# Optimization experiments

Hardware: AMD Instinct MI355X
Metric: run time of the kernel (lower is better)

## Reference

```python
import jax, jax.numpy as jnp
import numpy as np
from jax import lax

# Paraformer-large streaming decoder dims
L, H, DFF, NH, DK, K, V, T, S, CKV, LB = 16, 512, 2048, 4, 128, 11, 8404, 64, 2048, 256, 256


def _ln(x, g, b, eps=1e-5):
    m = jnp.mean(x, axis=-1, keepdims=True)
    var = jnp.mean((x - m) ** 2, axis=-1, keepdims=True)
    return (x - m) * lax.rsqrt(var + eps) * g + b


def setup_inputs() -> dict:
    key = jax.random.key(0)
    ks = jax.random.split(key, 20)
    w = lambda k, shp: jax.random.normal(k, shp, jnp.float32) * 0.02
    return {
        "encoder_out": jax.random.normal(ks[0], (1, S, H), jnp.float32),
        "list_frame": jax.random.normal(ks[1], (1, T, H), jnp.float32),
        "fsmn_cache": jax.random.normal(ks[2], (L, 1, H, K - 1), jnp.float32),
        "key_cache": jax.random.normal(ks[3], (L, NH, DK, CKV), jnp.float32),
        "value_cache": jax.random.normal(ks[4], (L, NH, CKV, DK), jnp.float32),
        "norm1_g": jnp.ones((L, H)), "norm1_b": jnp.zeros((L, H)),
        "norm2_g": jnp.ones((L, H)), "norm2_b": jnp.zeros((L, H)),
        "norm3_g": jnp.ones((L, H)), "norm3_b": jnp.zeros((L, H)),
        "ffn_norm_g": jnp.ones((L, DFF)), "ffn_norm_b": jnp.zeros((L, DFF)),
        "w1": w(ks[5], (L, H, DFF)), "b1": jnp.zeros((L, DFF)),
        "w2": w(ks[6], (L, DFF, H)),  # bias-free in FunASR DecoderSANM
        "fsmn_w": w(ks[7], (L, H, K)),  # depthwise conv, groups=H, no bias
        "qw": w(ks[8], (L, H, H)), "qb": jnp.zeros((L, H)),
        "kvw": w(ks[9], (L, H, 2 * H)), "kvb": jnp.zeros((L, 2 * H)),
        "ow": w(ks[10], (L, H, H)), "ob": jnp.zeros((L, H)),
        "d3_norm1_g": jnp.ones((H,)), "d3_norm1_b": jnp.zeros((H,)),
        "d3_w1": w(ks[11], (H, DFF)), "d3_b1": jnp.zeros((DFF,)),
        "d3_ffn_norm_g": jnp.ones((DFF,)), "d3_ffn_norm_b": jnp.zeros((DFF,)),
        "d3_w2": w(ks[12], (DFF, H)),
        "after_norm_g": jnp.ones((H,)), "after_norm_b": jnp.zeros((H,)),
        "out_w": w(ks[13], (H, V)), "out_b": jnp.zeros((V,)),
        "list_frame_len": T,
    }


def reference(encoder_out, list_frame, fsmn_cache, key_cache, value_cache,
              norm1_g, norm1_b, norm2_g, norm2_b, norm3_g, norm3_b,
              ffn_norm_g, ffn_norm_b, w1, b1, w2, fsmn_w, qw, qb, kvw, kvb, ow, ob,
              d3_norm1_g, d3_norm1_b, d3_w1, d3_b1, d3_ffn_norm_g, d3_ffn_norm_b, d3_w2,
              after_norm_g, after_norm_b, out_w, out_b, list_frame_len):
    enc = encoder_out[0]  # [S, H]
    scale = DK ** -0.5

    def layer_fn(lf, p):
        (fc, kc, vc, n1g, n1b, n2g, n2b, n3g, n3b, fng, fnb,
         W1, B1, W2, FW, QW, QB, KVW, KVB, OW, OB) = p
        residual = lf
        y = _ln(lf, n1g, n1b)
        y = _ln(jax.nn.relu(y @ W1 + B1), fng, fnb) @ W2
        y = _ln(y, n2g, n2b)
        # cache concat; slice [look_back:] with look_back = -(K-1)-T keeps all K-1+T cols
        x_cat = jnp.concatenate([fc, jnp.swapaxes(y, 1, 2)], axis=-1)  # [1, H, K-1+T]
        conv = lax.conv_general_dilated(
            x_cat, FW[:, None, :], (1,), 'VALID',
            dimension_numbers=('NCH', 'OIH', 'NCH'), feature_group_count=H)  # [1, H, T]
        x = jnp.swapaxes(conv, 1, 2) + y + residual
        residual = x
        q = (_ln(x, n3g, n3b)[0] @ QW + QB).reshape(-1, NH, DK).transpose(1, 0, 2) * scale  # [h, T, dk]
        kv = enc @ KVW + KVB  # [S, 2H]
        k = kv[:, :H].reshape(-1, NH, DK).transpose(1, 2, 0)  # [h, dk, S]
        v = kv[:, H:].reshape(-1, NH, DK).transpose(1, 0, 2)  # [h, S, dk]
        k = jnp.concatenate([kc, k], axis=2)  # [h, dk, CKV+S]
        v = jnp.concatenate([vc, v], axis=1)  # [h, CKV+S, dk]
        attn = jax.nn.softmax(jnp.einsum('htd,hds->hts', q, k), axis=-1)
        ctx = jnp.einsum('hts,hsd->htd', attn, v).transpose(1, 0, 2).reshape(1, -1, H)
        lf = residual + ctx @ OW + OB
        return lf, (x_cat, k[:, :, -LB:], v[:, -LB:, :])

    layer_params = (fsmn_cache, key_cache, value_cache, norm1_g, norm1_b, norm2_g, norm2_b,
                    norm3_g, norm3_b, ffn_norm_g, ffn_norm_b, w1, b1, w2, fsmn_w,
                    qw, qb, kvw, kvb, ow, ob)
    lf, (save_fsmn, save_keys, save_values) = lax.scan(layer_fn, list_frame, layer_params)
    x = _ln(lf, d3_norm1_g, d3_norm1_b)
    x = _ln(jax.nn.relu(x @ d3_w1 + d3_b1), d3_ffn_norm_g, d3_ffn_norm_b) @ d3_w2
    logits = _ln(x, after_norm_g, after_norm_b) @ out_w + out_b
    max_logit_ids = jnp.argmax(logits, axis=-1).astype(jnp.int32)
    return save_fsmn, save_keys, save_values, max_logit_ids
```

## Files before the change

### kernel.cpp

```cpp
#include <hip/hip_runtime.h>

constexpr int LAY = 16, HID = 512, FF = 2048, NHD = 4, DKH = 128, KW = 11,
              VOC = 8404, TT = 64, SEQ = 2048, LBN = 256;

__global__ void diag_k(float* __restrict__ p, float v) { p[threadIdx.x] = v; }

__global__ __launch_bounds__(256) void redln_k(
    const float* __restrict__ P, int N, int nch,
    const float* __restrict__ bias, const float* __restrict__ res, int relu,
    const float* __restrict__ g, const float* __restrict__ b,
    float* __restrict__ out1, float* __restrict__ out2) {
  __shared__ float buf[2048];
  __shared__ float red[256];
  const int m = blockIdx.x, tid = threadIdx.x;
  float s = 0.f;
  for (int n = tid; n < N; n += 256) {
    const float* p = P + (size_t)m * N + n;
    float v = 0.f;
    for (int c = 0; c < nch; ++c) v += p[(size_t)c * 64 * N];
    if (bias) v += bias[n];
    if (res) v += res[(size_t)m * N + n];
    if (relu) v = fmaxf(v, 0.f);
    if (out1) out1[(size_t)m * N + n] = v;
    buf[n] = v; s += v;
  }
  red[tid] = s; __syncthreads();
  for (int st = 128; st > 0; st >>= 1) { if (tid < st) red[tid] += red[tid + st]; __syncthreads(); }
  const float mean = red[0] / N;
  __syncthreads();
  float vs = 0.f;
  for (int n = tid; n < N; n += 256) { float d = buf[n] - mean; vs += d * d; }
  red[tid] = vs; __syncthreads();
  for (int st = 128; st > 0; st >>= 1) { if (tid < st) red[tid] += red[tid + st]; __syncthreads(); }
  const float inv = rsqrtf(red[0] / N + 1e-5f);
  for (int n = tid; n < N; n += 256)
    out2[(size_t)m * N + n] = (buf[n] - mean) * inv * g[n] + b[n];
}

__global__ __launch_bounds__(256) void gemm_nn(
    const float* __restrict__ A, int lda, long sA,
    const float* __restrict__ B, int ldb, long sB,
    float* __restrict__ C, int ldc, long sC,
    const float* __restrict__ bias,
    const float* __restrict__ res, int ldres,
    int N, int Kd, int flags, int nch,
    float* __restrict__ part, long pzs, int coff,
    int aCh, long aChS) {
  __shared__ float As[64][68];
  __shared__ float Bs[64][68];
  const int tid = threadIdx.x;
  const int lr = tid >> 4, lc = tid & 15;
  const int bn = blockIdx.x * 64;
  const int chunk = blockIdx.y;
  const int z = blockIdx.z;
  A += (long)z * sA; B += (long)z * sB; C += (long)z * sC;
  float acc[4][4] = {};
  const int ktiles = Kd >> 6;
  for (int kt = chunk; kt < ktiles; kt += nch) {
    const int k0 = kt << 6;
    __syncthreads();
#pragma unroll
    for (int i = 0; i < 4; ++i) {
      const int r = lr + 16 * i;
      const float* ap = A + (size_t)r * lda + k0 + lc * 4;
      float4 av = *(const float4*)ap;
      for (int c = 1; c < aCh; ++c) {
        const float4 t2 = *(const float4*)(ap + (size_t)c * aChS);
        av.x += t2.x; av.y += t2.y; av.z += t2.z; av.w += t2.w;
      }
      As[lc * 4 + 0][r] = av.x; As[lc * 4 + 1][r] = av.y;
      As[lc * 4 + 2][r] = av.z; As[lc * 4 + 3][r] = av.w;
      const int n = bn + lc * 4;
      const float* bp = B + (size_t)(k0 + r) * ldb + n;
      float4 bv;
      if (n + 3 < N) bv = *(const float4*)bp;
      else {
        bv.x = (n + 0 < N) ? bp[0] : 0.f;
        bv.y = (n + 1 < N) ? bp[1] : 0.f;
        bv.z = (n + 2 < N) ? bp[2] : 0.f;
        bv.w = (n + 3 < N) ? bp[3] : 0.f;
      }
      *(float4*)(&Bs[r][lc * 4]) = bv;
    }
    __syncthreads();
#pragma unroll 8
    for (int kk = 0; kk < 64; ++kk) {
      const float4 a = *(const float4*)(&As[kk][lr * 4]);
      const float4 b = *(const float4*)(&Bs[kk][lc * 4]);
      acc[0][0] += a.x * b.x; acc[0][1] += a.x * b.y; acc[0][2] += a.x * b.z; acc[0][3] += a.x * b.w;
      acc[1][0] += a.y * b.x; acc[1][1] += a.y * b.y; acc[1][2] += a.y * b.z; acc[1][3] += a.y * b.w;
      acc[2][0] += a.z * b.x; acc[2][1] += a.z * b.y; acc[2][2] += a.z * b.z; acc[2][3] += a.z * b.w;
      acc[3][0] += a.w * b.x; acc[3][1] += a.w * b.y; acc[3][2] += a.w * b.z; acc[3][3] += a.w * b.w;
    }
  }
  if (part) {
    float* P = part + (size_t)z * pzs + (size_t)(coff + chunk) * 64 * N;
#pragma unroll
    for (int i = 0; i < 4; ++i) {
      const int m = lr * 4 + i;
#pragma unroll
      for (int j = 0; j < 4; ++j) P[(size_t)m * N + bn + lc * 4 + j] = acc[i][j];
    }
    return;
  }
#pragma unroll
  for (int i = 0; i < 4; ++i) {
    const int m = lr * 4 + i;
#pragma unroll
    for (int j = 0; j < 4; ++j) {
      const int n = bn + lc * 4 + j;
      if (n < N) {
        float v = acc[i][j];
        if (bias) v += bias[n];
        if (res) v += res[(size_t)m * ldres + n];
        if (flags & 2) v += C[(size_t)m * ldc + n];
        if (flags & 1) v = fmaxf(v, 0.f);
        C[(size_t)m * ldc + n] = v;
      }
    }
  }
}

__global__ __launch_bounds__(256) void red_k(
    const float* __restrict__ P, float* __restrict__ out,
    int N, int nch, long pzs, int outld, int zoff,
    const float* __restrict__ bias, const float* __restrict__ res,
    const float* __restrict__ rsv, const float* __restrict__ bvv,
    int relu, int total) {
  const int idx = blockIdx.x * 256 + threadIdx.x;
  if (idx >= total) return;
  const int z = idx / (64 * N);
  const int rem = idx - z * 64 * N;
  const int t = rem / N;
  const int n = rem - t * N;
  const float* p = P + (size_t)z * pzs + (size_t)t * N + n;
  float s = 0.f;
  for (int c = 0; c < nch; ++c) s += p[(size_t)c * 64 * N];
  const int oc = z * zoff + n;
  if (bias) s += bias[oc];
  if (res) s += res[(size_t)t * outld + oc];
  if (rsv) s += rsv[z * 64 + t] * bvv[oc];
  if (relu) s = fmaxf(s, 0.f);
  out[(size_t)t * outld + oc] = s;
}

__global__ __launch_bounds__(256) void gemm_nt(
    const float* __restrict__ A, int lda, long sA,
    const float* __restrict__ B, int ldb, long sB,
    float* __restrict__ C, int ldc, long sC,
    int N, int Kd) {
  __shared__ float As[64][68];
  __shared__ float Bs[64][68];
  const int tid = threadIdx.x;
  const int lr = tid >> 4, lc = tid & 15;
  const int bn = blockIdx.x * 64;
  const int z = blockIdx.z;
  A += (long)z * sA; B += (long)z * sB; C += (long)z * sC;
  float acc[4][4] = {};
  for (int k0 = 0; k0 < Kd; k0 += 64) {
    __syncthreads();
#pragma unroll
    for (int i = 0; i < 4; ++i) {
      const int r = lr + 16 * i;
      const float4 av = *(const float4*)(A + (size_t)r * lda + k0 + lc * 4);
      As[lc * 4 + 0][r] = av.x; As[lc * 4 + 1][r] = av.y;
      As[lc * 4 + 2][r] = av.z; As[lc * 4 + 3][r] = av.w;
      const float4 bv = *(const float4*)(B + (size_t)(bn + r) * ldb + k0 + lc * 4);
      Bs[lc * 4 + 0][r] = bv.x; Bs[lc * 4 + 1][r] = bv.y;
      Bs[lc * 4 + 2][r] = bv.z; Bs[lc * 4 + 3][r] = bv.w;
    }
    __syncthreads();
#pragma unroll 8
    for (int kk = 0; kk < 64; ++kk) {
      const float4 a = *(const float4*)(&As[kk][lr * 4]);
      const float4 b = *(const float4*)(&Bs[kk][lc * 4]);
      acc[0][0] += a.x * b.x; acc[0][1] += a.x * b.y; acc[0][2] += a.x * b.z; acc[0][3] += a.x * b.w;
      acc[1][0] += a.y * b.x; acc[1][1] += a.y * b.y; acc[1][2] += a.y * b.z; acc[1][3] += a.y * b.w;
      acc[2][0] += a.z * b.x; acc[2][1] += a.z * b.y; acc[2][2] += a.z * b.z; acc[2][3] += a.z * b.w;
      acc[3][0] += a.w * b.x; acc[3][1] += a.w * b.y; acc[3][2] += a.w * b.z; acc[3][3] += a.w * b.w;
    }
  }
#pragma unroll
  for (int i = 0; i < 4; ++i) {
    const int m = lr * 4 + i;
#pragma unroll
    for (int j = 0; j < 4; ++j) {
      const int n = bn + lc * 4 + j;
      C[(size_t)m * ldc + n] = acc[i][j];
    }
  }
}

__global__ __launch_bounds__(256) void attn1_k(
    const float* __restrict__ qbf, const float* __restrict__ Wkv,
    const float* __restrict__ kcl,
    float* __restrict__ qp, float* __restrict__ sc,
    int ckv, int sct) {
  __shared__ float As[64][68];
  __shared__ float Bs[64][68];
  const int tid = threadIdx.x;
  const int lr = tid >> 4, lc = tid & 15;
  const int h = blockIdx.z;
  const bool isQp = blockIdx.x < 8;
  const int bn = (isQp ? blockIdx.x : blockIdx.x - 8) * 64;
  const float* A = qbf + h * DKH;
  float acc[4][4] = {};
  for (int k0 = 0; k0 < DKH; k0 += 64) {
    __syncthreads();
#pragma unroll
    for (int i = 0; i < 4; ++i) {
      const int r = lr + 16 * i;
      const float4 av = *(const float4*)(A + (size_t)r * HID + k0 + lc * 4);
      As[lc * 4 + 0][r] = av.x; As[lc * 4 + 1][r] = av.y;
      As[lc * 4 + 2][r] = av.z; As[lc * 4 + 3][r] = av.w;
      if (isQp) {
        const float4 bv = *(const float4*)(Wkv + (size_t)(bn + r) * (2 * HID) + h * DKH + k0 + lc * 4);
        Bs[lc * 4 + 0][r] = bv.x; Bs[lc * 4 + 1][r] = bv.y;
        Bs[lc * 4 + 2][r] = bv.z; Bs[lc * 4 + 3][r] = bv.w;
      } else {
        const float4 bv = *(const float4*)(kcl + ((size_t)h * DKH + k0 + r) * ckv + bn + lc * 4);
        *(float4*)(&Bs[r][lc * 4]) = bv;
      }
    }
    __syncthreads();
#pragma unroll 8
    for (int kk = 0; kk < 64; ++kk) {
      const float4 a = *(const float4*)(&As[kk][lr * 4]);
      const float4 b = *(const float4*)(&Bs[kk][lc * 4]);
      acc[0][0] += a.x * b.x; acc[0][1] += a.x * b.y; acc[0][2] += a.x * b.z; acc[0][3] += a.x * b.w;
      acc[1][0] += a.y * b.x; acc[1][1] += a.y * b.y; acc[1][2] += a.y * b.z; acc[1][3] += a.y * b.w;
      acc[2][0] += a.z * b.x; acc[2][1] += a.z * b.y; acc[2][2] += a.z * b.z; acc[2][3] += a.z * b.w;
      acc[3][0] += a.w * b.x; acc[3][1] += a.w * b.y; acc[3][2] += a.w * b.z; acc[3][3] += a.w * b.w;
    }
  }
  if (isQp) {
    float* C = qp + (size_t)h * TT * HID;
#pragma unroll
    for (int i = 0; i < 4; ++i)
#pragma unroll
      for (int j = 0; j < 4; ++j)
        C[(size_t)(lr * 4 + i) * HID + bn + lc * 4 + j] = acc[i][j];
  } else {
    float* C = sc + (size_t)h * TT * sct;
#pragma unroll
    for (int i = 0; i < 4; ++i)
#pragma unroll
      for (int j = 0; j < 4; ++j)
        C[(size_t)(lr * 4 + i) * sct + bn + lc * 4 + j] = acc[i][j];
  }
}

__global__ __launch_bounds__(256) void attn2_k(
    const float* __restrict__ sc, const float* __restrict__ vcl,
    const float* __restrict__ enc,
    float* __restrict__ part, float* __restrict__ partE,
    int ckv, int sct, int ncho, long pzc) {
  __shared__ float As[64][68];
  __shared__ float Bs[64][68];
  const int tid = threadIdx.x;
  const int lr = tid >> 4, lc = tid & 15;
  const int h = blockIdx.z;
  const int by = blockIdx.y;
  const bool isOld = blockIdx.x < 2;
  if (isOld && by >= ncho) return;
  if (!isOld && by >= 4) return;
  const float* A;
  const float* Bb;
  int lda, ldb, N, ktiles, nch, bn;
  float* P;
  if (isOld) {
    A = sc + (size_t)h * TT * sct;  lda = sct;
    Bb = vcl + (size_t)h * ckv * DKH; ldb = DKH;
    N = DKH; ktiles = ckv >> 6; nch = ncho; bn = blockIdx.x * 64;
    P = part + (size_t)h * pzc + (size_t)by * 64 * DKH;
  } else {
    A = sc + ckv + (size_t)h * TT * sct; lda = sct;
    Bb = enc; ldb = HID;
    N = HID; ktiles = SEQ >> 6; nch = 4; bn = (blockIdx.x - 2) * 64;
    P = partE + (size_t)h * (4L * 64 * HID) + (size_t)by * 64 * HID;
  }
  float acc[4][4] = {};
  for (int kt = by; kt < ktiles; kt += nch) {
    const int k0 = kt << 6;
    __syncthreads();
#pragma unroll
    for (int i = 0; i < 4; ++i) {
      const int r = lr + 16 * i;
      const float4 av = *(const float4*)(A + (size_t)r * lda + k0 + lc * 4);
      As[lc * 4 + 0][r] = av.x; As[lc * 4 + 1][r] = av.y;
      As[lc * 4 + 2][r] = av.z; As[lc * 4 + 3][r] = av.w;
      const float4 bv = *(const float4*)(Bb + (size_t)(k0 + r) * ldb + bn + lc * 4);
      *(float4*)(&Bs[r][lc * 4]) = bv;
    }
    __syncthreads();
#pragma unroll 8
    for (int kk = 0; kk < 64; ++kk) {
      const float4 a = *(const float4*)(&As[kk][lr * 4]);
      const float4 b = *(const float4*)(&Bs[kk][lc * 4]);
      acc[0][0] += a.x * b.x; acc[0][1] += a.x * b.y; acc[0][2] += a.x * b.z; acc[0][3] += a.x * b.w;
      acc[1][0] += a.y * b.x; acc[1][1] += a.y * b.y; acc[1][2] += a.y * b.z; acc[1][3] += a.y * b.w;
      acc[2][0] += a.z * b.x; acc[2][1] += a.z * b.y; acc[2][2] += a.z * b.z; acc[2][3] += a.z * b.w;
      acc[3][0] += a.w * b.x; acc[3][1] += a.w * b.y; acc[3][2] += a.w * b.z; acc[3][3] += a.w * b.w;
    }
  }
#pragma unroll
  for (int i = 0; i < 4; ++i)
#pragma unroll
    for (int j = 0; j < 4; ++j)
      P[(size_t)(lr * 4 + i) * N + bn + lc * 4 + j] = acc[i][j];
}

__global__ __launch_bounds__(128) void fsmn_k(const float* __restrict__ y4,
                                              const float* __restrict__ lfin,
                                              const float* __restrict__ cache,
                                              const float* __restrict__ fw,
                                              float* __restrict__ xout,
                                              float* __restrict__ xcat_out) {
  __shared__ float xc[KW - 1 + TT];
  const int tid = threadIdx.x, h = blockIdx.x;
  if (tid < KW - 1) xc[tid] = cache[h * (KW - 1) + tid];
  else if (tid < KW - 1 + TT) xc[tid] = y4[(size_t)(tid - (KW - 1)) * HID + h];
  __syncthreads();
  if (tid < KW - 1 + TT) xcat_out[h * (KW - 1 + TT) + tid] = xc[tid];
  if (tid < TT) {
    float a = 0.f;
#pragma unroll
    for (int k = 0; k < KW; ++k) a += xc[tid + k] * fw[h * KW + k];
    const size_t o = (size_t)tid * HID + h;
    xout[o] = a + y4[o] + lfin[o];
  }
}

__global__ __launch_bounds__(256) void softmax_k(float* __restrict__ sc,
                                                 float* __restrict__ rs,
                                                 const float* __restrict__ qbf,
                                                 const float* __restrict__ kb,
                                                 int cols, int newStart, float alpha) {
  __shared__ float red[256];
  const int tid = threadIdx.x;
  const int row = blockIdx.x;
  const int h = row >> 6, t = row & 63;
  sc += (size_t)row * cols;
  float qv = 0.f;
  if (tid < DKH) qv = qbf[t * HID + h * DKH + tid] * kb[h * DKH + tid];
  red[tid] = qv; __syncthreads();
  for (int st = 64; st > 0; st >>= 1) { if (tid < st) red[tid] += red[tid + st]; __syncthreads(); }
  const float qcv = red[0];
  __syncthreads();
  float m = -3.4e38f;
  for (int c = tid; c < cols; c += 256) {
    float v = (sc[c] + (c >= newStart ? qcv : 0.f)) * alpha;
    m = fmaxf(m, v);
  }
  red[tid] = m; __syncthreads();
  for (int st = 128; st > 0; st >>= 1) { if (tid < st) red[tid] = fmaxf(red[tid], red[tid + st]); __syncthreads(); }
  m = red[0]; __syncthreads();
  float s = 0.f;
  for (int c = tid; c < cols; c += 256) {
    float v = (sc[c] + (c >= newStart ? qcv : 0.f)) * alpha;
    float e = __expf(v - m);
    sc[c] = e; s += e;
  }
  red[tid] = s; __syncthreads();
  for (int st = 128; st > 0; st >>= 1) { if (tid < st) red[tid] += red[tid + st]; __syncthreads(); }
  const float inv = 1.f / red[0];
  float ns = 0.f;
  for (int c = tid; c < cols; c += 256) {
    float p = sc[c] * inv; sc[c] = p;
    if (c >= newStart) ns += p;
  }
  __syncthreads();
  red[tid] = ns; __syncthreads();
  for (int st = 128; st > 0; st >>= 1) { if (tid < st) red[tid] += red[tid + st]; __syncthreads(); }
  if (tid == 0) rs[row] = red[0];
}

__global__ __launch_bounds__(256) void argmax_k(const float* __restrict__ lg,
                                                float* __restrict__ out) {
  __shared__ float vs[256];
  __shared__ int ix[256];
  const int tid = threadIdx.x;
  lg += (size_t)blockIdx.x * VOC;
  float bm = -3.4e38f;
  int bi = 0;
  for (int c = tid; c < VOC; c += 256) { float v = lg[c]; if (v > bm) { bm = v; bi = c; } }
  vs[tid] = bm; ix[tid] = bi; __syncthreads();
  for (int st = 128; st > 0; st >>= 1) {
    if (tid < st) {
      if (vs[tid + st] > vs[tid] || (vs[tid + st] == vs[tid] && ix[tid + st] < ix[tid])) {
        vs[tid] = vs[tid + st]; ix[tid] = ix[tid + st];
      }
    }
    __syncthreads();
  }
  if (tid == 0) out[blockIdx.x] = (float)ix[0];
}

__global__ __launch_bounds__(256) void kvsave_k(const float* __restrict__ enc,
                                                const float* __restrict__ kvw,
                                                const float* __restrict__ kvb,
                                                float* __restrict__ keys,
                                                float* __restrict__ vals) {
  __shared__ float As[64][68];
  __shared__ float Bs[64][68];
  const int tid = threadIdx.x;
  const int lr = tid >> 4, lc = tid & 15;
  const int bn = blockIdx.x * 64, bm = blockIdx.y * 64;
  const int l = blockIdx.z;
  const float* W = kvw + (size_t)l * HID * 2 * HID;
  float acc[4][4] = {};
  for (int k0 = 0; k0 < HID; k0 += 64) {
    __syncthreads();
#pragma unroll
    for (int i = 0; i < 4; ++i) {
      const int r = lr + 16 * i;
      const float4 av =
          *(const float4*)(enc + (size_t)(SEQ - LBN + bm + r) * HID + k0 + lc * 4);
      As[lc * 4 + 0][r] = av.x; As[lc * 4 + 1][r] = av.y;
      As[lc * 4 + 2][r] = av.z; As[lc * 4 + 3][r] = av.w;
      const float4 bv = *(const float4*)(W + (size_t)(k0 + r) * (2 * HID) + bn + lc * 4);
      *(float4*)(&Bs[r][lc * 4]) = bv;
    }
    __syncthreads();
#pragma unroll 8
    for (int kk = 0; kk < 64; ++kk) {
      const float4 a = *(const float4*)(&As[kk][lr * 4]);
      const float4 b = *(const float4*)(&Bs[kk][lc * 4]);
      acc[0][0] += a.x * b.x; acc[0][1] += a.x * b.y; acc[0][2] += a.x * b.z; acc[0][3] += a.x * b.w;
      acc[1][0] += a.y * b.x; acc[1][1] += a.y * b.y; acc[1][2] += a.y * b.z; acc[1][3] += a.y * b.w;
      acc[2][0] += a.z * b.x; acc[2][1] += a.z * b.y; acc[2][2] += a.z * b.z; acc[2][3] += a.z * b.w;
      acc[3][0] += a.w * b.x; acc[3][1] += a.w * b.y; acc[3][2] += a.w * b.z; acc[3][3] += a.w * b.w;
    }
  }
#pragma unroll
  for (int i = 0; i < 4; ++i) {
    const int m = bm + lr * 4 + i;
#pragma unroll
    for (int j = 0; j < 4; ++j) {
      const int n = bn + lc * 4 + j;
      const float v = acc[i][j] + kvb[(size_t)l * 2 * HID + n];
      if (n < 512) {
        const int h = n >> 7, d = n & 127;
        keys[(((size_t)l * NHD + h) * DKH + d) * LBN + m] = v;
      } else {
        const int c = n - 512, h = c >> 7, d = c & 127;
        vals[(((size_t)l * NHD + h) * LBN + m) * DKH + d] = v;
      }
    }
  }
}

extern "C" void kernel_launch(void* const* d_in, const int* in_sizes, int n_in,
                              void* d_out, int out_size, void* d_ws, size_t ws_size,
                              hipStream_t stream) {
  static const int EXPECT[34] = {
      1048576, 32768, 81920, -1, -1,
      8192, 8192, 8192, 8192, 8192, 8192,
      32768, 32768,
      16777216, 32768, 16777216, 90112,
      4194304, 8192, 8388608, 16384, 4194304, 8192,
      512, 512, 1048576, 2048, 2048, 2048, 1048576,
      512, 512, 4302848, 8404};
  if (out_size != 4800576) {
    diag_k<<<1, 64, 0, stream>>>((float*)d_out, 9800000.f);
    return;
  }
  float* out_fsmn = (float*)d_out;
  float* out_keys = out_fsmn + (size_t)LAY * HID * (KW - 1 + TT);
  float* out_vals = out_keys + (size_t)LAY * NHD * DKH * LBN;
  float* out_ids  = out_vals + (size_t)LAY * NHD * LBN * DKH;
  if (n_in < 34) {
    diag_k<<<1, 64, 0, stream>>>(out_ids, 9900000.f);
    return;
  }
  for (int i = 0; i < 34; ++i) {
    if (EXPECT[i] >= 0 && in_sizes[i] != EXPECT[i]) {
      diag_k<<<1, 64, 0, stream>>>(out_ids, (float)((i + 1) * 100000));
      return;
    }
  }
  const long per = (long)LAY * NHD * DKH;
  const long ckl = (long)in_sizes[3] / per;
  if ((long)in_sizes[3] != ckl * per || in_sizes[4] != in_sizes[3] ||
      ckl <= 0 || (ckl & 63) != 0 || ckl > 6144) {
    diag_k<<<1, 64, 0, stream>>>(out_fsmn, (float)in_sizes[3]);
    return;
  }
  const int ckv = (int)ckl;
  const int sct = ckv + SEQ;
  const long TS = (long)TT * sct;
  const int ncho = (ckv / 64 < 8) ? (ckv / 64) : 8;

  const float* enc    = (const float*)d_in[0];
  const float* lfrm   = (const float*)d_in[1];
  const float* fcache = (const float*)d_in[2];
  const float* kcache = (const float*)d_in[3];
  const float* vcache = (const float*)d_in[4];
  const float* n1g = (const float*)d_in[5];  const float* n1b = (const float*)d_in[6];
  const float* n2g = (const float*)d_in[7];  const float* n2b = (const float*)d_in[8];
  const float* n3g = (const float*)d_in[9];  const float* n3b = (const float*)d_in[10];
  const float* fng = (const float*)d_in[11]; const float* fnb = (const float*)d_in[12];
  const float* w1  = (const float*)d_in[13]; const float* b1  = (const float*)d_in[14];
  const float* w2  = (const float*)d_in[15];
  const float* fw  = (const float*)d_in[16];
  const float* qw  = (const float*)d_in[17]; const float* qbi  = (const float*)d_in[18];
  const float* kvw = (const float*)d_in[19]; const float* kvbi = (const float*)d_in[20];
  const float* ow  = (const float*)d_in[21]; const float* obi  = (const float*)d_in[22];
  const float* d3n1g = (const float*)d_in[23]; const float* d3n1b = (const float*)d_in[24];
  const float* d3w1  = (const float*)d_in[25]; const float* d3b1  = (const float*)d_in[26];
  const float* d3fng = (const float*)d_in[27]; const float* d3fnb = (const float*)d_in[28];
  const float* d3w2  = (const float*)d_in[29];
  const float* ang   = (const float*)d_in[30]; const float* anb = (const float*)d_in[31];
  const float* outw  = (const float*)d_in[32]; const float* outb = (const float*)d_in[33];

  float* sc  = out_keys;
  float* ov  = out_vals;
  float* lf  = ov + 0;
  float* y1  = ov + 32768;
  float* y4  = ov + 98304;
  float* xb  = ov + 131072;
  float* qbf = ov + 163840;
  float* ctx = ov + 196608;
  float* y2  = ov + 360448;
  float* qp  = ov + 491520;
  float* rs  = ov + 753920;
  float* lg  = ov + 754176;
  float* partE = lg;
  float* part  = ov + 1292032;

  const float alpha = 0.08838834764831845f;
  const long TH = (long)TT * HID;
  const long pz_ctx = (long)(ncho + 4) * 64 * DKH;

  redln_k<<<TT, 256, 0, stream>>>(lfrm, HID, 1, nullptr, nullptr, 0,
                                  n1g, n1b, lf, y1);

  for (int l = 0; l < LAY; ++l) {
    const float* Wkv = kvw + (size_t)l * HID * 2 * HID;
    const float* Bkv = kvbi + (size_t)l * 2 * HID;
    gemm_nn<<<dim3(32, 4, 1), 256, 0, stream>>>(
        y1, HID, 0, w1 + (size_t)l * HID * FF, FF, 0, nullptr, 0, 0,
        nullptr, nullptr, 0, FF, HID, 0, 4, part, 0, 0, 1, 0);
    redln_k<<<TT, 256, 0, stream>>>(part, FF, 4, b1 + (size_t)l * FF, nullptr, 1,
                                    fng + (size_t)l * FF, fnb + (size_t)l * FF,
                                    nullptr, y2);
    gemm_nn<<<dim3(8, 16, 1), 256, 0, stream>>>(
        y2, FF, 0, w2 + (size_t)l * FF * HID, HID, 0, nullptr, 0, 0,
        nullptr, nullptr, 0, HID, FF, 0, 16, part, 0, 0, 1, 0);
    redln_k<<<TT, 256, 0, stream>>>(part, HID, 16, nullptr, nullptr, 0,
                                    n2g + l * HID, n2b + l * HID, nullptr, y4);
    fsmn_k<<<HID, 128, 0, stream>>>(y4, lf, fcache + (size_t)l * HID * (KW - 1),
                                    fw + (size_t)l * HID * KW, xb,
                                    out_fsmn + (size_t)l * HID * (KW - 1 + TT));
    redln_k<<<TT, 256, 0, stream>>>(xb, HID, 1, nullptr, nullptr, 0,
                                    n3g + l * HID, n3b + l * HID, nullptr, y1);
    gemm_nn<<<dim3(8, 8, 1), 256, 0, stream>>>(
        y1, HID, 0, qw + (size_t)l * HID * HID, HID, 0, nullptr, 0, 0,
        nullptr, nullptr, 0, HID, HID, 0, 8, part, 0, 0, 1, 0);
    red_k<<<128, 256, 0, stream>>>(part, qbf, HID, 8, 0, HID, HID,
                                   qbi + (size_t)l * HID, nullptr, nullptr, nullptr,
                                   0, TT * HID);
    attn1_k<<<dim3(8 + ckv / 64, 1, NHD), 256, 0, stream>>>(
        qbf, Wkv, kcache + (size_t)l * NHD * DKH * ckv, qp, sc, ckv, sct);
    gemm_nt<<<dim3(32, 1, NHD), 256, 0, stream>>>(
        qp, HID, TH, enc, HID, 0, sc + ckv, sct, TS, SEQ, HID);
    softmax_k<<<NHD * TT, 256, 0, stream>>>(sc, rs, qbf, Bkv, sct, ckv, alpha);
    attn2_k<<<dim3(10, (ncho > 4 ? ncho : 4), NHD), 256, 0, stream>>>(
        sc, vcache + (size_t)l * NHD * ckv * DKH, enc, part, partE,
        ckv, sct, ncho, pz_ctx);
    gemm_nn<<<dim3(2, 4, NHD), 256, 0, stream>>>(
        partE, HID, 4L * 64 * HID, Wkv + HID, 2 * HID, DKH, nullptr, 0, 0,
        nullptr, nullptr, 0, DKH, HID, 0, 4, part, pz_ctx, ncho, 4, 64L * HID);
    red_k<<<128, 256, 0, stream>>>(part, ctx, DKH, ncho + 4, pz_ctx, HID, DKH,
                                   nullptr, nullptr, rs, Bkv + HID, 0, NHD * TT * DKH);
    gemm_nn<<<dim3(8, 8, 1), 256, 0, stream>>>(
        ctx, HID, 0, ow + (size_t)l * HID * HID, HID, 0, nullptr, 0, 0,
        nullptr, nullptr, 0, HID, HID, 0, 8, part, 0, 0, 1, 0);
    const float* ng = (l + 1 < LAY) ? n1g + (l + 1) * HID : d3n1g;
    const float* nb = (l + 1 < LAY) ? n1b + (l + 1) * HID : d3n1b;
    redln_k<<<TT, 256, 0, stream>>>(part, HID, 8, obi + (size_t)l * HID, xb, 0,
                                    ng, nb, lf, y1);
  }

  gemm_nn<<<dim3(32, 4, 1), 256, 0, stream>>>(
      y1, HID, 0, d3w1, FF, 0, nullptr, 0, 0, nullptr, nullptr, 0,
      FF, HID, 0, 4, part, 0, 0, 1, 0);
  redln_k<<<TT, 256, 0, stream>>>(part, FF, 4, d3b1, nullptr, 1,
                                  d3fng, d3fnb, nullptr, y2);
  gemm_nn<<<dim3(8, 16, 1), 256, 0, stream>>>(
      y2, FF, 0, d3w2, HID, 0, nullptr, 0, 0, nullptr, nullptr, 0,
      HID, FF, 0, 16, part, 0, 0, 1, 0);
  redln_k<<<TT, 256, 0, stream>>>(part, HID, 16, nullptr, nullptr, 0,
                                  ang, anb, nullptr, y4);
  gemm_nn<<<dim3((VOC + 63) / 64, 1, 1), 256, 0, stream>>>(
      y4, HID, 0, outw, VOC, 0, lg, VOC, 0, outb, nullptr, 0,
      VOC, HID, 0, 1, nullptr, 0, 0, 1, 0);
  argmax_k<<<TT, 256, 0, stream>>>(lg, out_ids);

  kvsave_k<<<dim3(2 * HID / 64, LBN / 64, LAY), 256, 0, stream>>>(
      enc, kvw, kvbi, out_keys, out_vals);
}
```

Measured before the change: 2.985 ms.

## Prefetch GEMM tiles into registers and fuse fsmn/LN and q-bias reduction

Adds register-level prefetch of the next K tile in the gemm_nn, gemm_nt, attn1 and attn2 kernels so global loads overlap with the FMA loop. Fuses the FSMN depthwise conv with the following layernorm into one per-row kernel. Drops the separate q-bias reduction kernel by summing the split-K partials inside attn1 and softmax. Softmax now caches its scaled row in shared memory to avoid re-reading global memory. The cost is more registers and redundant q-partial summation across blocks.

```diff
diff --git a/kernel.cpp b/kernel.cpp
--- a/kernel.cpp
+++ b/kernel.cpp
@@ -56,9 +56,10 @@
   A += (long)z * sA; B += (long)z * sB; C += (long)z * sC;
   float acc[4][4] = {};
   const int ktiles = Kd >> 6;
-  for (int kt = chunk; kt < ktiles; kt += nch) {
+  float4 pa[4], pb[4];
+  int kt = chunk;
+  if (kt < ktiles) {
     const int k0 = kt << 6;
-    __syncthreads();
 #pragma unroll
     for (int i = 0; i < 4; ++i) {
       const int r = lr + 16 * i;
@@ -68,8 +69,7 @@
         const float4 t2 = *(const float4*)(ap + (size_t)c * aChS);
         av.x += t2.x; av.y += t2.y; av.z += t2.z; av.w += t2.w;
       }
-      As[lc * 4 + 0][r] = av.x; As[lc * 4 + 1][r] = av.y;
-      As[lc * 4 + 2][r] = av.z; As[lc * 4 + 3][r] = av.w;
+      pa[i] = av;
       const int n = bn + lc * 4;
       const float* bp = B + (size_t)(k0 + r) * ldb + n;
       float4 bv;
@@ -80,9 +80,44 @@
         bv.z = (n + 2 < N) ? bp[2] : 0.f;
         bv.w = (n + 3 < N) ? bp[3] : 0.f;
       }
-      *(float4*)(&Bs[r][lc * 4]) = bv;
-    }
-    __syncthreads();
+      pb[i] = bv;
+    }
+  }
+  while (kt < ktiles) {
+#pragma unroll
+    for (int i = 0; i < 4; ++i) {
+      const int r = lr + 16 * i;
+      As[lc * 4 + 0][r] = pa[i].x; As[lc * 4 + 1][r] = pa[i].y;
+      As[lc * 4 + 2][r] = pa[i].z; As[lc * 4 + 3][r] = pa[i].w;
+      *(float4*)(&Bs[r][lc * 4]) = pb[i];
+    }
+    const int ktn = kt + nch;
+    __syncthreads();
+    if (ktn < ktiles) {
+      const int k0 = ktn << 6;
+#pragma unroll
+      for (int i = 0; i < 4; ++i) {
+        const int r = lr + 16 * i;
+        const float* ap = A + (size_t)r * lda + k0 + lc * 4;
+        float4 av = *(const float4*)ap;
+        for (int c = 1; c < aCh; ++c) {
+          const float4 t2 = *(const float4*)(ap + (size_t)c * aChS);
+          av.x += t2.x; av.y += t2.y; av.z += t2.z; av.w += t2.w;
+        }
+        pa[i] = av;
+        const int n = bn + lc * 4;
+        const float* bp = B + (size_t)(k0 + r) * ldb + n;
+        float4 bv;
+        if (n + 3 < N) bv = *(const float4*)bp;
+        else {
+          bv.x = (n + 0 < N) ? bp[0] : 0.f;
+          bv.y = (n + 1 < N) ? bp[1] : 0.f;
+          bv.z = (n + 2 < N) ? bp[2] : 0.f;
+          bv.w = (n + 3 < N) ? bp[3] : 0.f;
+        }
+        pb[i] = bv;
+      }
+    }
 #pragma unroll 8
     for (int kk = 0; kk < 64; ++kk) {
       const float4 a = *(const float4*)(&As[kk][lr * 4]);
@@ -92,6 +127,8 @@
       acc[2][0] += a.z * b.x; acc[2][1] += a.z * b.y; acc[2][2] += a.z * b.z; acc[2][3] += a.z * b.w;
       acc[3][0] += a.w * b.x; acc[3][1] += a.w * b.y; acc[3][2] += a.w * b.z; acc[3][3] += a.w * b.w;
     }
+    __syncthreads();
+    kt = ktn;
   }
   if (part) {
     float* P = part + (size_t)z * pzs + (size_t)(coff + chunk) * 64 * N;
@@ -157,19 +194,35 @@
   const int z = blockIdx.z;
   A += (long)z * sA; B += (long)z * sB; C += (long)z * sC;
   float acc[4][4] = {};
-  for (int k0 = 0; k0 < Kd; k0 += 64) {
-    __syncthreads();
-#pragma unroll
-    for (int i = 0; i < 4; ++i) {
-      const int r = lr + 16 * i;
-      const float4 av = *(const float4*)(A + (size_t)r * lda + k0 + lc * 4);
-      As[lc * 4 + 0][r] = av.x; As[lc * 4 + 1][r] = av.y;
-      As[lc * 4 + 2][r] = av.z; As[lc * 4 + 3][r] = av.w;
-      const float4 bv = *(const float4*)(B + (size_t)(bn + r) * ldb + k0 + lc * 4);
-      Bs[lc * 4 + 0][r] = bv.x; Bs[lc * 4 + 1][r] = bv.y;
-      Bs[lc * 4 + 2][r] = bv.z; Bs[lc * 4 + 3][r] = bv.w;
-    }
-    __syncthreads();
+  const int ktiles = Kd >> 6;
+  float4 pa[4], pb[4];
+  {
+#pragma unroll
+    for (int i = 0; i < 4; ++i) {
+      const int r = lr + 16 * i;
+      pa[i] = *(const float4*)(A + (size_t)r * lda + lc * 4);
+      pb[i] = *(const float4*)(B + (size_t)(bn + r) * ldb + lc * 4);
+    }
+  }
+  for (int kt = 0; kt < ktiles; ++kt) {
+#pragma unroll
+    for (int i = 0; i < 4; ++i) {
+      const int r = lr + 16 * i;
+      As[lc * 4 + 0][r] = pa[i].x; As[lc * 4 + 1][r] = pa[i].y;
+      As[lc * 4 + 2][r] = pa[i].z; As[lc * 4 + 3][r] = pa[i].w;
+      Bs[lc * 4 + 0][r] = pb[i].x; Bs[lc * 4 + 1][r] = pb[i].y;
+      Bs[lc * 4 + 2][r] = pb[i].z; Bs[lc * 4 + 3][r] = pb[i].w;
+    }
+    __syncthreads();
+    if (kt + 1 < ktiles) {
+      const int k0 = (kt + 1) << 6;
+#pragma unroll
+      for (int i = 0; i < 4; ++i) {
+        const int r = lr + 16 * i;
+        pa[i] = *(const float4*)(A + (size_t)r * lda + k0 + lc * 4);
+        pb[i] = *(const float4*)(B + (size_t)(bn + r) * ldb + k0 + lc * 4);
+      }
+    }
 #pragma unroll 8
     for (int kk = 0; kk < 64; ++kk) {
       const float4 a = *(const float4*)(&As[kk][lr * 4]);
@@ -179,6 +232,7 @@
       acc[2][0] += a.z * b.x; acc[2][1] += a.z * b.y; acc[2][2] += a.z * b.z; acc[2][3] += a.z * b.w;
       acc[3][0] += a.w * b.x; acc[3][1] += a.w * b.y; acc[3][2] += a.w * b.z; acc[3][3] += a.w * b.w;
     }
+    __syncthreads();
   }
 #pragma unroll
   for (int i = 0; i < 4; ++i) {
@@ -192,8 +246,8 @@
 }
 
 __global__ __launch_bounds__(256) void attn1_k(
-    const float* __restrict__ qbf, const float* __restrict__ Wkv,
-    const float* __restrict__ kcl,
+    const float* __restrict__ qpart, const float* __restrict__ qbi_l,
+    const float* __restrict__ Wkv, const float* __restrict__ kcl,
     float* __restrict__ qp, float* __restrict__ sc,
     int ckv, int sct) {
   __shared__ float As[64][68];
@@ -203,26 +257,61 @@
   const int h = blockIdx.z;
   const bool isQp = blockIdx.x < 8;
   const int bn = (isQp ? blockIdx.x : blockIdx.x - 8) * 64;
-  const float* A = qbf + h * DKH;
   float acc[4][4] = {};
-  for (int k0 = 0; k0 < DKH; k0 += 64) {
-    __syncthreads();
-#pragma unroll
-    for (int i = 0; i < 4; ++i) {
-      const int r = lr + 16 * i;
-      const float4 av = *(const float4*)(A + (size_t)r * HID + k0 + lc * 4);
-      As[lc * 4 + 0][r] = av.x; As[lc * 4 + 1][r] = av.y;
-      As[lc * 4 + 2][r] = av.z; As[lc * 4 + 3][r] = av.w;
+  float4 pa[4], pb[4];
+  {
+#pragma unroll
+    for (int i = 0; i < 4; ++i) {
+      const int r = lr + 16 * i;
+      const float* ap = qpart + (size_t)r * HID + h * DKH + lc * 4;
+      float4 av = *(const float4*)ap;
+      for (int c = 1; c < 8; ++c) {
+        const float4 t2 = *(const float4*)(ap + (size_t)c * 64 * HID);
+        av.x += t2.x; av.y += t2.y; av.z += t2.z; av.w += t2.w;
+      }
+      const float4 bb = *(const float4*)(qbi_l + h * DKH + lc * 4);
+      av.x += bb.x; av.y += bb.y; av.z += bb.z; av.w += bb.w;
+      pa[i] = av;
+      if (isQp)
+        pb[i] = *(const float4*)(Wkv + (size_t)(bn + r) * (2 * HID) + h * DKH + lc * 4);
+      else
+        pb[i] = *(const float4*)(kcl + ((size_t)h * DKH + r) * ckv + bn + lc * 4);
+    }
+  }
+  for (int kt = 0; kt < 2; ++kt) {
+#pragma unroll
+    for (int i = 0; i < 4; ++i) {
+      const int r = lr + 16 * i;
+      As[lc * 4 + 0][r] = pa[i].x; As[lc * 4 + 1][r] = pa[i].y;
+      As[lc * 4 + 2][r] = pa[i].z; As[lc * 4 + 3][r] = pa[i].w;
       if (isQp) {
-        const float4 bv = *(const float4*)(Wkv + (size_t)(bn + r) * (2 * HID) + h * DKH + k0 + lc * 4);
-        Bs[lc * 4 + 0][r] = bv.x; Bs[lc * 4 + 1][r] = bv.y;
-        Bs[lc * 4 + 2][r] = bv.z; Bs[lc * 4 + 3][r] = bv.w;
+        Bs[lc * 4 + 0][r] = pb[i].x; Bs[lc * 4 + 1][r] = pb[i].y;
+        Bs[lc * 4 + 2][r] = pb[i].z; Bs[lc * 4 + 3][r] = pb[i].w;
       } else {
-        const float4 bv = *(const float4*)(kcl + ((size_t)h * DKH + k0 + r) * ckv + bn + lc * 4);
-        *(float4*)(&Bs[r][lc * 4]) = bv;
-      }
-    }
-    __syncthreads();
+        *(float4*)(&Bs[r][lc * 4]) = pb[i];
+      }
+    }
+    __syncthreads();
+    if (kt == 0) {
+      const int k0 = 64;
+#pragma unroll
+      for (int i = 0; i < 4; ++i) {
+        const int r = lr + 16 * i;
+        const float* ap = qpart + (size_t)r * HID + h * DKH + k0 + lc * 4;
+        float4 av = *(const float4*)ap;
+        for (int c = 1; c < 8; ++c) {
+          const float4 t2 = *(const float4*)(ap + (size_t)c * 64 * HID);
+          av.x += t2.x; av.y += t2.y; av.z += t2.z; av.w += t2.w;
+        }
+        const float4 bb = *(const float4*)(qbi_l + h * DKH + k0 + lc * 4);
+        av.x += bb.x; av.y += bb.y; av.z += bb.z; av.w += bb.w;
+        pa[i] = av;
+        if (isQp)
+          pb[i] = *(const float4*)(Wkv + (size_t)(bn + r) * (2 * HID) + h * DKH + k0 + lc * 4);
+        else
+          pb[i] = *(const float4*)(kcl + ((size_t)h * DKH + k0 + r) * ckv + bn + lc * 4);
+      }
+    }
 #pragma unroll 8
     for (int kk = 0; kk < 64; ++kk) {
       const float4 a = *(const float4*)(&As[kk][lr * 4]);
@@ -232,6 +321,7 @@
       acc[2][0] += a.z * b.x; acc[2][1] += a.z * b.y; acc[2][2] += a.z * b.z; acc[2][3] += a.z * b.w;
       acc[3][0] += a.w * b.x; acc[3][1] += a.w * b.y; acc[3][2] += a.w * b.z; acc[3][3] += a.w * b.w;
     }
+    __syncthreads();
   }
   if (isQp) {
     float* C = qp + (size_t)h * TT * HID;
@@ -280,19 +370,36 @@
     P = partE + (size_t)h * (4L * 64 * HID) + (size_t)by * 64 * HID;
   }
   float acc[4][4] = {};
-  for (int kt = by; kt < ktiles; kt += nch) {
+  float4 pa[4], pb[4];
+  int kt = by;
+  if (kt < ktiles) {
     const int k0 = kt << 6;
-    __syncthreads();
-#pragma unroll
-    for (int i = 0; i < 4; ++i) {
-      const int r = lr + 16 * i;
-      const float4 av = *(const float4*)(A + (size_t)r * lda + k0 + lc * 4);
-      As[lc * 4 + 0][r] = av.x; As[lc * 4 + 1][r] = av.y;
-      As[lc * 4 + 2][r] = av.z; As[lc * 4 + 3][r] = av.w;
-      const float4 bv = *(const float4*)(Bb + (size_t)(k0 + r) * ldb + bn + lc * 4);
-      *(float4*)(&Bs[r][lc * 4]) = bv;
-    }
-    __syncthreads();
+#pragma unroll
+    for (int i = 0; i < 4; ++i) {
+      const int r = lr + 16 * i;
+      pa[i] = *(const float4*)(A + (size_t)r * lda + k0 + lc * 4);
+      pb[i] = *(const float4*)(Bb + (size_t)(k0 + r) * ldb + bn + lc * 4);
+    }
+  }
+  while (kt < ktiles) {
+#pragma unroll
+    for (int i = 0; i < 4; ++i) {
+      const int r = lr + 16 * i;
+      As[lc * 4 + 0][r] = pa[i].x; As[lc * 4 + 1][r] = pa[i].y;
+      As[lc * 4 + 2][r] = pa[i].z; As[lc * 4 + 3][r] = pa[i].w;
+      *(float4*)(&Bs[r][lc * 4]) = pb[i];
+    }
+    const int ktn = kt + nch;
+    __syncthreads();
+    if (ktn < ktiles) {
+      const int k0 = ktn << 6;
+#pragma unroll
+      for (int i = 0; i < 4; ++i) {
+        const int r = lr + 16 * i;
+        pa[i] = *(const float4*)(A + (size_t)r * lda + k0 + lc * 4);
+        pb[i] = *(const float4*)(Bb + (size_t)(k0 + r) * ldb + bn + lc * 4);
+      }
+    }
 #pragma unroll 8
     for (int kk = 0; kk < 64; ++kk) {
       const float4 a = *(const float4*)(&As[kk][lr * 4]);
@@ -302,6 +409,8 @@
       acc[2][0] += a.z * b.x; acc[2][1] += a.z * b.y; acc[2][2] += a.z * b.z; acc[2][3] += a.z * b.w;
       acc[3][0] += a.w * b.x; acc[3][1] += a.w * b.y; acc[3][2] += a.w * b.z; acc[3][3] += a.w * b.w;
     }
+    __syncthreads();
+    kt = ktn;
   }
 #pragma unroll
   for (int i = 0; i < 4; ++i)
@@ -310,63 +419,90 @@
       P[(size_t)(lr * 4 + i) * N + bn + lc * 4 + j] = acc[i][j];
 }
 
-__global__ __launch_bounds__(128) void fsmn_k(const float* __restrict__ y4,
-                                              const float* __restrict__ lfin,
-                                              const float* __restrict__ cache,
-                                              const float* __restrict__ fw,
-                                              float* __restrict__ xout,
-                                              float* __restrict__ xcat_out) {
-  __shared__ float xc[KW - 1 + TT];
-  const int tid = threadIdx.x, h = blockIdx.x;
-  if (tid < KW - 1) xc[tid] = cache[h * (KW - 1) + tid];
-  else if (tid < KW - 1 + TT) xc[tid] = y4[(size_t)(tid - (KW - 1)) * HID + h];
+__global__ __launch_bounds__(256) void fsmnln_k(
+    const float* __restrict__ y4, const float* __restrict__ lfin,
+    const float* __restrict__ cache, const float* __restrict__ fw,
+    const float* __restrict__ g, const float* __restrict__ b,
+    float* __restrict__ xb, float* __restrict__ xcat,
+    float* __restrict__ y1out) {
+  __shared__ float buf[HID];
+  __shared__ float red[256];
+  const int t = blockIdx.x, tid = threadIdx.x;
+  float s = 0.f;
+  for (int h = tid; h < HID; h += 256) {
+    float conv = 0.f;
+#pragma unroll
+    for (int k = 0; k < KW; ++k) {
+      const int j = t + k;
+      const float xcv = (j < KW - 1) ? cache[h * (KW - 1) + j]
+                                     : y4[(size_t)(j - (KW - 1)) * HID + h];
+      conv += xcv * fw[h * KW + k];
+    }
+    const float yv = y4[(size_t)t * HID + h];
+    const float x = conv + yv + lfin[(size_t)t * HID + h];
+    xb[(size_t)t * HID + h] = x;
+    buf[h] = x; s += x;
+    xcat[h * (KW - 1 + TT) + (KW - 1) + t] = yv;
+    if (t == 0) {
+      for (int j2 = 0; j2 < KW - 1; ++j2)
+        xcat[h * (KW - 1 + TT) + j2] = cache[h * (KW - 1) + j2];
+    }
+  }
+  red[tid] = s; __syncthreads();
+  for (int st = 128; st > 0; st >>= 1) { if (tid < st) red[tid] += red[tid + st]; __syncthreads(); }
+  const float mean = red[0] / HID;
   __syncthreads();
-  if (tid < KW - 1 + TT) xcat_out[h * (KW - 1 + TT) + tid] = xc[tid];
-  if (tid < TT) {
-    float a = 0.f;
-#pragma unroll
-    for (int k = 0; k < KW; ++k) a += xc[tid + k] * fw[h * KW + k];
-    const size_t o = (size_t)tid * HID + h;
-    xout[o] = a + y4[o] + lfin[o];
-  }
-}
-
-__global__ __launch_bounds__(256) void softmax_k(float* __restrict__ sc,
-                                                 float* __restrict__ rs,
-                                                 const float* __restrict__ qbf,
-                                                 const float* __restrict__ kb,
-                                                 int cols, int newStart, float alpha) {
+  float vs = 0.f;
+  for (int h = tid; h < HID; h += 256) { float d = buf[h] - mean; vs += d * d; }
+  red[tid] = vs; __syncthreads();
+  for (int st = 128; st > 0; st >>= 1) { if (tid < st) red[tid] += red[tid + st]; __syncthreads(); }
+  const float inv = rsqrtf(red[0] / HID + 1e-5f);
+  for (int h = tid; h < HID; h += 256)
+    y1out[(size_t)t * HID + h] = (buf[h] - mean) * inv * g[h] + b[h];
+}
+
+__global__ __launch_bounds__(256) void softmax_k(
+    float* __restrict__ sc, float* __restrict__ rs,
+    const float* __restrict__ qpart, const float* __restrict__ qbi_l,
+    const float* __restrict__ kb,
+    int cols, int newStart, float alpha) {
+  __shared__ float srow[8192];
   __shared__ float red[256];
   const int tid = threadIdx.x;
   const int row = blockIdx.x;
   const int h = row >> 6, t = row & 63;
   sc += (size_t)row * cols;
   float qv = 0.f;
-  if (tid < DKH) qv = qbf[t * HID + h * DKH + tid] * kb[h * DKH + tid];
+  if (tid < DKH) {
+    const float* qp0 = qpart + (size_t)t * HID + h * DKH + tid;
+    float q = qp0[0];
+    for (int c = 1; c < 8; ++c) q += qp0[(size_t)c * 64 * HID];
+    q += qbi_l[h * DKH + tid];
+    qv = q * kb[h * DKH + tid];
+  }
   red[tid] = qv; __syncthreads();
   for (int st = 64; st > 0; st >>= 1) { if (tid < st) red[tid] += red[tid + st]; __syncthreads(); }
   const float qcv = red[0];
   __syncthreads();
   float m = -3.4e38f;
   for (int c = tid; c < cols; c += 256) {
-    float v = (sc[c] + (c >= newStart ? qcv : 0.f)) * alpha;
-    m = fmaxf(m, v);
+    const float v = (sc[c] + (c >= newStart ? qcv : 0.f)) * alpha;
+    srow[c] = v; m = fmaxf(m, v);
   }
   red[tid] = m; __syncthreads();
   for (int st = 128; st > 0; st >>= 1) { if (tid < st) red[tid] = fmaxf(red[tid], red[tid + st]); __syncthreads(); }
   m = red[0]; __syncthreads();
   float s = 0.f;
   for (int c = tid; c < cols; c += 256) {
-    float v = (sc[c] + (c >= newStart ? qcv : 0.f)) * alpha;
-    float e = __expf(v - m);
-    sc[c] = e; s += e;
+    const float e = __expf(srow[c] - m);
+    srow[c] = e; s += e;
   }
   red[tid] = s; __syncthreads();
   for (int st = 128; st > 0; st >>= 1) { if (tid < st) red[tid] += red[tid + st]; __syncthreads(); }
   const float inv = 1.f / red[0];
   float ns = 0.f;
   for (int c = tid; c < cols; c += 256) {
-    float p = sc[c] * inv; sc[c] = p;
+    const float p = srow[c] * inv; sc[c] = p;
     if (c >= newStart) ns += p;
   }
   __syncthreads();
@@ -519,7 +655,6 @@
   float* y1  = ov + 32768;
   float* y4  = ov + 98304;
   float* xb  = ov + 131072;
-  float* qbf = ov + 163840;
   float* ctx = ov + 196608;
   float* y2  = ov + 360448;
   float* qp  = ov + 491520;
@@ -538,6 +673,7 @@
   for (int l = 0; l < LAY; ++l) {
     const float* Wkv = kvw + (size_t)l * HID * 2 * HID;
     const float* Bkv = kvbi + (size_t)l * 2 * HID;
+    const float* qbi_l = qbi + (size_t)l * HID;
     gemm_nn<<<dim3(32, 4, 1), 256, 0, stream>>>(
         y1, HID, 0, w1 + (size_t)l * HID * FF, FF, 0, nullptr, 0, 0,
         nullptr, nullptr, 0, FF, HID, 0, 4, part, 0, 0, 1, 0);
@@ -549,22 +685,18 @@
         nullptr, nullptr, 0, HID, FF, 0, 16, part, 0, 0, 1, 0);
     redln_k<<<TT, 256, 0, stream>>>(part, HID, 16, nullptr, nullptr, 0,
                                     n2g + l * HID, n2b + l * HID, nullptr, y4);
-    fsmn_k<<<HID, 128, 0, stream>>>(y4, lf, fcache + (size_t)l * HID * (KW - 1),
-                                    fw + (size_t)l * HID * KW, xb,
-                                    out_fsmn + (size_t)l * HID * (KW - 1 + TT));
-    redln_k<<<TT, 256, 0, stream>>>(xb, HID, 1, nullptr, nullptr, 0,
-                                    n3g + l * HID, n3b + l * HID, nullptr, y1);
+    fsmnln_k<<<TT, 256, 0, stream>>>(y4, lf, fcache + (size_t)l * HID * (KW - 1),
+                                     fw + (size_t)l * HID * KW,
+                                     n3g + l * HID, n3b + l * HID,
+                                     xb, out_fsmn + (size_t)l * HID * (KW - 1 + TT), y1);
     gemm_nn<<<dim3(8, 8, 1), 256, 0, stream>>>(
         y1, HID, 0, qw + (size_t)l * HID * HID, HID, 0, nullptr, 0, 0,
         nullptr, nullptr, 0, HID, HID, 0, 8, part, 0, 0, 1, 0);
-    red_k<<<128, 256, 0, stream>>>(part, qbf, HID, 8, 0, HID, HID,
-                                   qbi + (size_t)l * HID, nullptr, nullptr, nullptr,
-                                   0, TT * HID);
     attn1_k<<<dim3(8 + ckv / 64, 1, NHD), 256, 0, stream>>>(
-        qbf, Wkv, kcache + (size_t)l * NHD * DKH * ckv, qp, sc, ckv, sct);
+        part, qbi_l, Wkv, kcache + (size_t)l * NHD * DKH * ckv, qp, sc, ckv, sct);
     gemm_nt<<<dim3(32, 1, NHD), 256, 0, stream>>>(
         qp, HID, TH, enc, HID, 0, sc + ckv, sct, TS, SEQ, HID);
-    softmax_k<<<NHD * TT, 256, 0, stream>>>(sc, rs, qbf, Bkv, sct, ckv, alpha);
+    softmax_k<<<NHD * TT, 256, 0, stream>>>(sc, rs, part, qbi_l, Bkv, sct, ckv, alpha);
     attn2_k<<<dim3(10, (ncho > 4 ? ncho : 4), NHD), 256, 0, stream>>>(
         sc, vcache + (size_t)l * NHD * ckv * DKH, enc, part, partE,
         ckv, sct, ncho, pz_ctx);
```

Measured after the change: 3.027 ms. About the same (+1.4%).
